# Kernel tuning notes

Hardware: AMD Instinct MI355X
Metric: run time of the kernel (lower is better)

Reference implementation:

```python
import jax, jax.numpy as jnp
import numpy as np

N = 50000   # nodes
E = 800000  # edges (avg degree 16)
IN = 3      # in_feats = value(1) + u(2)
H = 128     # hid_feats


def setup_inputs() -> dict:
    key = jax.random.key(0)
    ks = jax.random.split(key, 24)
    value = jax.random.normal(ks[0], (N, 1), jnp.float32)
    u = jax.random.normal(ks[1], (N, 2), jnp.float32)
    src = jax.random.randint(ks[2], (E,), 0, N, dtype=jnp.int32)
    dst = jax.random.randint(ks[3], (E,), 0, N, dtype=jnp.int32)
    dims = [IN, H // 2, H, H, H, H, H, H, H, H, 1]
    inp = {"value": value, "u": u, "src": src, "dst": dst}
    for i in range(10):
        inp[f"W{i+1}"] = jax.random.normal(ks[4 + i], (dims[i], dims[i + 1]), jnp.float32) / np.sqrt(dims[i]).astype(np.float32)
        inp[f"b{i+1}"] = jnp.zeros((dims[i + 1],), jnp.float32)
    return inp


def _gconv(x, src, dst, inv_deg, W, b):
    # DGL GraphConv norm='right': sum incoming src features, divide by in-degree, linear, bias
    agg = jax.ops.segment_sum(x[src], dst, num_segments=N)  # [N, d_in]
    return (agg * inv_deg) @ W + b


def reference(value, u, src, dst, W1, b1, W2, b2, W3, b3, W4, b4, W5, b5,
              W6, b6, W7, b7, W8, b8, W9, b9, W10, b10):
    deg = jax.ops.segment_sum(jnp.ones((E,), jnp.float32), dst, num_segments=N)
    inv_deg = (1.0 / jnp.clip(deg, 1.0))[:, None]  # DGL clamps in-degree to >=1
    lrelu = lambda h: jax.nn.leaky_relu(h, 0.01)
    x = jnp.concatenate([value, u], axis=1)  # [N, 3]
    h = _gconv(x, src, dst, inv_deg, W1, b1)
    h = lrelu(_gconv(h, src, dst, inv_deg, W2, b2))
    h = lrelu(_gconv(h, src, dst, inv_deg, W3, b3))
    h = lrelu(_gconv(h, src, dst, inv_deg, W4, b4))
    h = _gconv(h, src, dst, inv_deg, W5, b5)
    h = _gconv(h, src, dst, inv_deg, W6, b6)
    h = _gconv(h, src, dst, inv_deg, W7, b7)
    h = _gconv(h, src, dst, inv_deg, W8, b8)
    h = jax.nn.sigmoid(_gconv(h, src, dst, inv_deg, W9, b9))
    h = _gconv(h, src, dst, inv_deg, W10, b10)  # [N, 1]
    return h
```

## Files before the change

### kernel.cpp

```cpp
#include <hip/hip_runtime.h>
#include <math.h>

typedef unsigned int u32;
typedef unsigned short u16;
using bf16x8 = __attribute__((ext_vector_type(8))) short;
using f32x4 = __attribute__((ext_vector_type(4))) float;

__device__ inline float bf_lo(u32 v) { return __uint_as_float(v << 16); }
__device__ inline float bf_hi(u32 v) { return __uint_as_float(v & 0xFFFF0000u); }
__device__ inline u16 f2bf(float f) {
    u32 u = __float_as_uint(f);
    return (u16)((u + 0x7FFFu + ((u >> 16) & 1u)) >> 16);
}
__device__ inline float bf2f(u16 h) { return __uint_as_float((u32)h << 16); }
__device__ inline float invdeg(int d) { return 1.0f / (float)(d > 1 ? d : 1); }

#define BIN_SHIFT 13

__global__ __launch_bounds__(256) void k_scatter_seq(const int* __restrict__ src,
                                                     const int* __restrict__ dst,
                                                     int* __restrict__ cur,
                                                     u16* __restrict__ colp,
                                                     int E, int EB) {
    const int bin = blockIdx.x / EB;
    int e = (blockIdx.x - bin * EB) * 256 + threadIdx.x;
    if (e >= E) return;
    int d = dst[e];
    if ((d >> BIN_SHIFT) != bin) return;
    int slot = atomicAdd(&cur[d], 1);
    if (slot < 64) colp[(size_t)d * 64 + slot] = (u16)src[e];
}

__global__ __launch_bounds__(256) void k_x4(const float* __restrict__ value,
                                            const float* __restrict__ u,
                                            float4* __restrict__ x4, int n) {
    int i = blockIdx.x * 256 + threadIdx.x;
    if (i < n) x4[i] = make_float4(value[i], u[2 * i], u[2 * i + 1], 0.f);
}

struct W7 { const float* p[7]; };

__global__ __launch_bounds__(256) void k_pack(W7 wp, const float* __restrict__ W64,
                                              u16* __restrict__ hi128, u16* __restrict__ lo128,
                                              u16* __restrict__ hi64, u16* __restrict__ lo64) {
    const int l = blockIdx.y;
    if (l < 7) {
        const float* W = wp.p[l];
        int g = blockIdx.x * 256 + threadIdx.x;
        int ct = g >> 8;
        int rem = g & 255;
        int ks = rem >> 6;
        int lane = rem & 63;
        int kbase = ks * 32 + ((lane >> 4) << 3);
        int n = (ct << 4) + (lane & 15);
        size_t off = ((size_t)l * 2048 + g) * 8;
#pragma unroll
        for (int j = 0; j < 8; ++j) {
            float w = W[(size_t)(kbase + j) * 128 + n];
            u16 h = f2bf(w);
            hi128[off + j] = h;
            lo128[off + j] = f2bf(w - bf2f(h));
        }
    } else {
        if (blockIdx.x >= 4) return;
        int g = blockIdx.x * 256 + threadIdx.x;
        int ct = g >> 7;
        int rem = g & 127;
        int ks = rem >> 6;
        int lane = rem & 63;
        int kbase = ks * 32 + ((lane >> 4) << 3);
        int n = (ct << 4) + (lane & 15);
        size_t off = (size_t)g * 8;
#pragma unroll
        for (int j = 0; j < 8; ++j) {
            float w = W64[(size_t)(kbase + j) * 128 + n];
            u16 h = f2bf(w);
            hi64[off + j] = h;
            lo64[off + j] = f2bf(w - bf2f(h));
        }
    }
}

__global__ __launch_bounds__(256) void k_l1(const float4* __restrict__ x4,
                                            const u16* __restrict__ colp,
                                            const int* __restrict__ deg,
                                            const float* __restrict__ W1,
                                            const float* __restrict__ b1,
                                            u16* __restrict__ out, int nNodes) {
    const int lane = threadIdx.x & 63;
    const int n = blockIdx.x * 4 + (threadIdx.x >> 6);
    if (n >= nNodes) return;
    int dfull = deg[n];
    int dg = dfull > 64 ? 64 : dfull;
    const u16* cl = colp + (size_t)n * 64;
    float a0 = 0.f, a1 = 0.f, a2 = 0.f;
    if (lane < dg) {
        float4 v = x4[cl[lane]];
        a0 = v.x; a1 = v.y; a2 = v.z;
    }
#pragma unroll
    for (int o = 32; o; o >>= 1) {
        a0 += __shfl_xor(a0, o, 64);
        a1 += __shfl_xor(a1, o, 64);
        a2 += __shfl_xor(a2, o, 64);
    }
    float iv = invdeg(dfull);
    float y = b1[lane] + iv * (a0 * W1[lane] + a1 * W1[64 + lane] + a2 * W1[128 + lane]);
    out[(size_t)n * 64 + lane] = f2bf(y);
}

__global__ __launch_bounds__(256) void k_agg128b(const u32* __restrict__ H32,
                                                 const u16* __restrict__ colp,
                                                 const int* __restrict__ deg,
                                                 u32* __restrict__ out, int nNodes) {
    const int lane = threadIdx.x & 63;
    const int n = blockIdx.x * 4 + (threadIdx.x >> 6);
    if (n >= nNodes) return;
    int dfull = deg[n];
    int dg = dfull > 64 ? 64 : dfull;
    const u16* cl = colp + (size_t)n * 64;
    int myc = (lane < dg) ? (int)cl[lane] : 0;
    float a0 = 0.f, a1 = 0.f, b0 = 0.f, b1 = 0.f;
    int j = 0;
    for (; j + 8 <= dg; j += 8) {
        u32 v0 = H32[(size_t)__builtin_amdgcn_readlane(myc, j + 0) * 64 + lane];
        u32 v1 = H32[(size_t)__builtin_amdgcn_readlane(myc, j + 1) * 64 + lane];
        u32 v2 = H32[(size_t)__builtin_amdgcn_readlane(myc, j + 2) * 64 + lane];
        u32 v3 = H32[(size_t)__builtin_amdgcn_readlane(myc, j + 3) * 64 + lane];
        u32 v4 = H32[(size_t)__builtin_amdgcn_readlane(myc, j + 4) * 64 + lane];
        u32 v5 = H32[(size_t)__builtin_amdgcn_readlane(myc, j + 5) * 64 + lane];
        u32 v6 = H32[(size_t)__builtin_amdgcn_readlane(myc, j + 6) * 64 + lane];
        u32 v7 = H32[(size_t)__builtin_amdgcn_readlane(myc, j + 7) * 64 + lane];
        a0 += bf_lo(v0) + bf_lo(v1) + bf_lo(v2) + bf_lo(v3);
        a1 += bf_hi(v0) + bf_hi(v1) + bf_hi(v2) + bf_hi(v3);
        b0 += bf_lo(v4) + bf_lo(v5) + bf_lo(v6) + bf_lo(v7);
        b1 += bf_hi(v4) + bf_hi(v5) + bf_hi(v6) + bf_hi(v7);
    }
    for (; j + 4 <= dg; j += 4) {
        u32 v0 = H32[(size_t)__builtin_amdgcn_readlane(myc, j + 0) * 64 + lane];
        u32 v1 = H32[(size_t)__builtin_amdgcn_readlane(myc, j + 1) * 64 + lane];
        u32 v2 = H32[(size_t)__builtin_amdgcn_readlane(myc, j + 2) * 64 + lane];
        u32 v3 = H32[(size_t)__builtin_amdgcn_readlane(myc, j + 3) * 64 + lane];
        a0 += bf_lo(v0) + bf_lo(v1);
        a1 += bf_hi(v0) + bf_hi(v1);
        b0 += bf_lo(v2) + bf_lo(v3);
        b1 += bf_hi(v2) + bf_hi(v3);
    }
    for (; j < dg; ++j) {
        u32 v = H32[(size_t)__builtin_amdgcn_readlane(myc, j) * 64 + lane];
        a0 += bf_lo(v);
        a1 += bf_hi(v);
    }
    float iv = invdeg(dfull);
    out[(size_t)n * 64 + lane] =
        (u32)f2bf((a0 + b0) * iv) | ((u32)f2bf((a1 + b1) * iv) << 16);
}

__global__ __launch_bounds__(256) void k_agg64b(const u16* __restrict__ H16,
                                                const u16* __restrict__ colp,
                                                const int* __restrict__ deg,
                                                u16* __restrict__ out, int nNodes) {
    const int lane = threadIdx.x & 63;
    const int n = blockIdx.x * 4 + (threadIdx.x >> 6);
    if (n >= nNodes) return;
    int dfull = deg[n];
    int dg = dfull > 64 ? 64 : dfull;
    const u16* cl = colp + (size_t)n * 64;
    int myc = (lane < dg) ? (int)cl[lane] : 0;
    float a0 = 0.f, a1 = 0.f, b0 = 0.f, b1 = 0.f;
    int j = 0;
    for (; j + 8 <= dg; j += 8) {
        u16 v0 = H16[(size_t)__builtin_amdgcn_readlane(myc, j + 0) * 64 + lane];
        u16 v1 = H16[(size_t)__builtin_amdgcn_readlane(myc, j + 1) * 64 + lane];
        u16 v2 = H16[(size_t)__builtin_amdgcn_readlane(myc, j + 2) * 64 + lane];
        u16 v3 = H16[(size_t)__builtin_amdgcn_readlane(myc, j + 3) * 64 + lane];
        u16 v4 = H16[(size_t)__builtin_amdgcn_readlane(myc, j + 4) * 64 + lane];
        u16 v5 = H16[(size_t)__builtin_amdgcn_readlane(myc, j + 5) * 64 + lane];
        u16 v6 = H16[(size_t)__builtin_amdgcn_readlane(myc, j + 6) * 64 + lane];
        u16 v7 = H16[(size_t)__builtin_amdgcn_readlane(myc, j + 7) * 64 + lane];
        a0 += bf2f(v0) + bf2f(v1);
        a1 += bf2f(v2) + bf2f(v3);
        b0 += bf2f(v4) + bf2f(v5);
        b1 += bf2f(v6) + bf2f(v7);
    }
    for (; j + 4 <= dg; j += 4) {
        u16 v0 = H16[(size_t)__builtin_amdgcn_readlane(myc, j + 0) * 64 + lane];
        u16 v1 = H16[(size_t)__builtin_amdgcn_readlane(myc, j + 1) * 64 + lane];
        u16 v2 = H16[(size_t)__builtin_amdgcn_readlane(myc, j + 2) * 64 + lane];
        u16 v3 = H16[(size_t)__builtin_amdgcn_readlane(myc, j + 3) * 64 + lane];
        a0 += bf2f(v0) + bf2f(v1);
        b0 += bf2f(v2) + bf2f(v3);
    }
    for (; j < dg; ++j) {
        a0 += bf2f(H16[(size_t)__builtin_amdgcn_readlane(myc, j) * 64 + lane]);
    }
    out[(size_t)n * 64 + lane] = f2bf((a0 + a1 + b0 + b1) * invdeg(dfull));
}

template <int ACT>
__device__ inline float actf(float x) {
    if (ACT == 1) return x > 0.f ? x : 0.01f * x;
    if (ACT == 2) return 1.f / (1.f + expf(-x));
    return x;
}

template <int DIN, int ACT>
__global__ __launch_bounds__(256) void k_mm(const u16* __restrict__ A,
                                            const u16* __restrict__ pkHi,
                                            const u16* __restrict__ pkLo,
                                            const float* __restrict__ B,
                                            u16* __restrict__ Y, int nNodes) {
    constexpr int NKS = DIN / 32;
    const int lane = threadIdx.x & 63;
    const int w = threadIdx.x >> 6;
    const int base = blockIdx.x * 64 + w * 16;
    const int m = lane & 15;
    const int kb = lane >> 4;
    int arow = base + m;
    if (arow >= nNodes) arow = nNodes - 1;

    bf16x8 aF[NKS];
#pragma unroll
    for (int ks = 0; ks < NKS; ++ks)
        aF[ks] = *reinterpret_cast<const bf16x8*>(A + (size_t)arow * DIN + ks * 32 + kb * 8);

    const bf16x8* bh = reinterpret_cast<const bf16x8*>(pkHi);
    const bf16x8* bl = reinterpret_cast<const bf16x8*>(pkLo);

#pragma unroll
    for (int ct = 0; ct < 8; ++ct) {
        f32x4 acc = {0.f, 0.f, 0.f, 0.f};
#pragma unroll
        for (int ks = 0; ks < NKS; ++ks) {
            acc = __builtin_amdgcn_mfma_f32_16x16x32_bf16(aF[ks], bh[(ct * NKS + ks) * 64 + lane], acc, 0, 0, 0);
            acc = __builtin_amdgcn_mfma_f32_16x16x32_bf16(aF[ks], bl[(ct * NKS + ks) * 64 + lane], acc, 0, 0, 0);
        }
        float bias = B[ct * 16 + m];
#pragma unroll
        for (int r = 0; r < 4; ++r) {
            int row = base + kb * 4 + r;
            if (row < nNodes)
                Y[(size_t)row * 128 + ct * 16 + m] = f2bf(actf<ACT>(acc[r] + bias));
        }
    }
}

__global__ __launch_bounds__(256) void k_mm_last(const u16* __restrict__ A,
                                                 const u16* __restrict__ pkHi,
                                                 const u16* __restrict__ pkLo,
                                                 const float* __restrict__ B,
                                                 const float* __restrict__ w10,
                                                 float* __restrict__ t, int nNodes) {
    const int lane = threadIdx.x & 63;
    const int w = threadIdx.x >> 6;
    const int base = blockIdx.x * 64 + w * 16;
    const int m = lane & 15;
    const int kb = lane >> 4;
    int arow = base + m;
    if (arow >= nNodes) arow = nNodes - 1;

    bf16x8 aF[4];
#pragma unroll
    for (int ks = 0; ks < 4; ++ks)
        aF[ks] = *reinterpret_cast<const bf16x8*>(A + (size_t)arow * 128 + ks * 32 + kb * 8);

    const bf16x8* bh = reinterpret_cast<const bf16x8*>(pkHi);
    const bf16x8* bl = reinterpret_cast<const bf16x8*>(pkLo);

    float p0 = 0.f, p1 = 0.f, p2 = 0.f, p3 = 0.f;
#pragma unroll
    for (int ct = 0; ct < 8; ++ct) {
        f32x4 acc = {0.f, 0.f, 0.f, 0.f};
#pragma unroll
        for (int ks = 0; ks < 4; ++ks) {
            acc = __builtin_amdgcn_mfma_f32_16x16x32_bf16(aF[ks], bh[(ct * 4 + ks) * 64 + lane], acc, 0, 0, 0);
            acc = __builtin_amdgcn_mfma_f32_16x16x32_bf16(aF[ks], bl[(ct * 4 + ks) * 64 + lane], acc, 0, 0, 0);
        }
        float bias = B[ct * 16 + m];
        float wv = w10[ct * 16 + m];
        p0 += wv * actf<2>(acc[0] + bias);
        p1 += wv * actf<2>(acc[1] + bias);
        p2 += wv * actf<2>(acc[2] + bias);
        p3 += wv * actf<2>(acc[3] + bias);
    }
#pragma unroll
    for (int o = 1; o < 16; o <<= 1) {
        p0 += __shfl_xor(p0, o, 64);
        p1 += __shfl_xor(p1, o, 64);
        p2 += __shfl_xor(p2, o, 64);
        p3 += __shfl_xor(p3, o, 64);
    }
    if (m == 0) {
        int r0 = base + kb * 4;
        if (r0 + 0 < nNodes) t[r0 + 0] = p0;
        if (r0 + 1 < nNodes) t[r0 + 1] = p1;
        if (r0 + 2 < nNodes) t[r0 + 2] = p2;
        if (r0 + 3 < nNodes) t[r0 + 3] = p3;
    }
}

__global__ __launch_bounds__(256) void k_aggs(const float* __restrict__ t,
                                              const u16* __restrict__ colp,
                                              const int* __restrict__ deg,
                                              const float* __restrict__ B,
                                              float* __restrict__ out, int nNodes) {
    int n = blockIdx.x * 256 + threadIdx.x;
    if (n >= nNodes) return;
    int dfull = deg[n];
    int dg = dfull > 64 ? 64 : dfull;
    const u16* cl = colp + (size_t)n * 64;
    float s = 0.f;
    for (int j = 0; j < dg; ++j) s += t[cl[j]];
    out[n] = s * invdeg(dfull) + B[0];
}

extern "C" void kernel_launch(void* const* d_in, const int* in_sizes, int n_in,
                              void* d_out, int out_size, void* d_ws, size_t ws_size,
                              hipStream_t stream) {
    const float* value = (const float*)d_in[0];
    const float* u = (const float*)d_in[1];
    const int* src = (const int*)d_in[2];
    const int* dst = (const int*)d_in[3];
    const float* W[10];
    const float* b[10];
    for (int i = 0; i < 10; ++i) {
        W[i] = (const float*)d_in[4 + 2 * i];
        b[i] = (const float*)d_in[5 + 2 * i];
    }
    const int N = in_sizes[0];
    const int E = in_sizes[2];
    float* out = (float*)d_out;

    char* p = (char*)d_ws;
    auto carve = [&](size_t bytes) {
        char* r = p;
        p += (bytes + 255) & ~(size_t)255;
        return r;
    };
    int* deg = (int*)carve((size_t)N * 4);
    u16* colp = (u16*)carve((size_t)N * 64 * 2);
    float4* x4 = (float4*)carve((size_t)N * 16);
    u16* hA = (u16*)carve((size_t)N * 128 * 2);
    u16* hB = (u16*)carve((size_t)N * 128 * 2);
    u16* agg = (u16*)carve((size_t)N * 128 * 2);
    float* t10 = (float*)carve((size_t)N * 4);
    u16* pk128hi = (u16*)carve((size_t)7 * 2048 * 8 * 2);
    u16* pk128lo = (u16*)carve((size_t)7 * 2048 * 8 * 2);
    u16* pk64hi = (u16*)carve((size_t)1024 * 8 * 2);
    u16* pk64lo = (u16*)carve((size_t)1024 * 8 * 2);

    const int nbins = (N + (1 << BIN_SHIFT) - 1) >> BIN_SHIFT;
    const int EB = (E + 255) / 256;

    hipMemsetAsync(deg, 0, (size_t)N * 4, stream);
    k_scatter_seq<<<EB * nbins, 256, 0, stream>>>(src, dst, deg, colp, E, EB);
    k_x4<<<(N + 255) / 256, 256, 0, stream>>>(value, u, x4, N);

    W7 wp;
    for (int i = 0; i < 7; ++i) wp.p[i] = W[2 + i];
    k_pack<<<dim3(8, 8), 256, 0, stream>>>(wp, W[1], pk128hi, pk128lo, pk64hi, pk64lo);

    const int gw = (N + 3) / 4;
    const int gg = (N + 63) / 64;
    const int gt = (N + 255) / 256;
    const size_t PK = 2048 * 8;

    k_l1<<<gw, 256, 0, stream>>>(x4, colp, deg, W[0], b[0], hA, N);
    k_agg64b<<<gw, 256, 0, stream>>>(hA, colp, deg, agg, N);
    k_mm<64, 1><<<gg, 256, 0, stream>>>(agg, pk64hi, pk64lo, b[1], hB, N);
    k_agg128b<<<gw, 256, 0, stream>>>((const u32*)hB, colp, deg, (u32*)agg, N);
    k_mm<128, 1><<<gg, 256, 0, stream>>>(agg, pk128hi + 0 * PK, pk128lo + 0 * PK, b[2], hA, N);
    k_agg128b<<<gw, 256, 0, stream>>>((const u32*)hA, colp, deg, (u32*)agg, N);
    k_mm<128, 1><<<gg, 256, 0, stream>>>(agg, pk128hi + 1 * PK, pk128lo + 1 * PK, b[3], hB, N);
    k_agg128b<<<gw, 256, 0, stream>>>((const u32*)hB, colp, deg, (u32*)agg, N);
    k_mm<128, 0><<<gg, 256, 0, stream>>>(agg, pk128hi + 2 * PK, pk128lo + 2 * PK, b[4], hA, N);
    k_agg128b<<<gw, 256, 0, stream>>>((const u32*)hA, colp, deg, (u32*)agg, N);
    k_mm<128, 0><<<gg, 256, 0, stream>>>(agg, pk128hi + 3 * PK, pk128lo + 3 * PK, b[5], hB, N);
    k_agg128b<<<gw, 256, 0, stream>>>((const u32*)hB, colp, deg, (u32*)agg, N);
    k_mm<128, 0><<<gg, 256, 0, stream>>>(agg, pk128hi + 4 * PK, pk128lo + 4 * PK, b[6], hA, N);
    k_agg128b<<<gw, 256, 0, stream>>>((const u32*)hA, colp, deg, (u32*)agg, N);
    k_mm<128, 0><<<gg, 256, 0, stream>>>(agg, pk128hi + 5 * PK, pk128lo + 5 * PK, b[7], hB, N);
    k_agg128b<<<gw, 256, 0, stream>>>((const u32*)hB, colp, deg, (u32*)agg, N);
    k_mm_last<<<gg, 256, 0, stream>>>(agg, pk128hi + 6 * PK, pk128lo + 6 * PK, b[8], W[9], t10, N);
    k_aggs<<<gt, 256, 0, stream>>>(t10, colp, deg, b[9], out, N);
}
```

Before: 427.1 us.

## Fuse neighbor aggregation with MFMA matmul per 64-node tile and merge setup kernels

Each hidden layer now runs one 1024-thread block per 64-node tile. The block gathers and averages the neighbor features into the shared agg buffer, synchronises, then runs the split-bf16 MFMA matmul, with each wave computing two output column tiles. The edge scatter, input packing and weight packing kernels are merged into one front kernel to cut launches. The fused kernel still writes agg to global memory and reads it back after the block barrier, so traffic is barely reduced. It also puts a barrier between the gather and matmul phases, which limits overlap inside a block.

```diff
diff --git a/kernel.cpp b/kernel.cpp
--- a/kernel.cpp
+++ b/kernel.cpp
@@ -17,63 +17,67 @@
 
 #define BIN_SHIFT 13
 
-__global__ __launch_bounds__(256) void k_scatter_seq(const int* __restrict__ src,
-                                                     const int* __restrict__ dst,
-                                                     int* __restrict__ cur,
-                                                     u16* __restrict__ colp,
-                                                     int E, int EB) {
-    const int bin = blockIdx.x / EB;
-    int e = (blockIdx.x - bin * EB) * 256 + threadIdx.x;
-    if (e >= E) return;
-    int d = dst[e];
-    if ((d >> BIN_SHIFT) != bin) return;
-    int slot = atomicAdd(&cur[d], 1);
-    if (slot < 64) colp[(size_t)d * 64 + slot] = (u16)src[e];
-}
-
-__global__ __launch_bounds__(256) void k_x4(const float* __restrict__ value,
-                                            const float* __restrict__ u,
-                                            float4* __restrict__ x4, int n) {
-    int i = blockIdx.x * 256 + threadIdx.x;
-    if (i < n) x4[i] = make_float4(value[i], u[2 * i], u[2 * i + 1], 0.f);
-}
-
 struct W7 { const float* p[7]; };
 
-__global__ __launch_bounds__(256) void k_pack(W7 wp, const float* __restrict__ W64,
-                                              u16* __restrict__ hi128, u16* __restrict__ lo128,
-                                              u16* __restrict__ hi64, u16* __restrict__ lo64) {
-    const int l = blockIdx.y;
-    if (l < 7) {
+__global__ __launch_bounds__(256) void k_front(const int* __restrict__ src,
+                                               const int* __restrict__ dst,
+                                               int* __restrict__ cur,
+                                               u16* __restrict__ colp,
+                                               int E, int EB, int SB,
+                                               const float* __restrict__ value,
+                                               const float* __restrict__ u,
+                                               float4* __restrict__ x4, int n, int NBx4,
+                                               W7 wp, const float* __restrict__ W64,
+                                               u16* __restrict__ hi128, u16* __restrict__ lo128,
+                                               u16* __restrict__ hi64, u16* __restrict__ lo64) {
+    int blk = blockIdx.x;
+    if (blk < SB) {
+        const int bin = blk / EB;
+        int e = (blk - bin * EB) * 256 + threadIdx.x;
+        if (e >= E) return;
+        int d = dst[e];
+        if ((d >> BIN_SHIFT) != bin) return;
+        int slot = atomicAdd(&cur[d], 1);
+        if (slot < 64) colp[(size_t)d * 64 + slot] = (u16)src[e];
+        return;
+    }
+    int pb = blk - SB;
+    if (pb < NBx4) {
+        int i = pb * 256 + threadIdx.x;
+        if (i < n) x4[i] = make_float4(value[i], u[2 * i], u[2 * i + 1], 0.f);
+        return;
+    }
+    pb -= NBx4;
+    if (pb < 56) {
+        const int l = pb >> 3;
         const float* W = wp.p[l];
-        int g = blockIdx.x * 256 + threadIdx.x;
+        int g = (pb & 7) * 256 + threadIdx.x;
         int ct = g >> 8;
         int rem = g & 255;
         int ks = rem >> 6;
         int lane = rem & 63;
         int kbase = ks * 32 + ((lane >> 4) << 3);
-        int n = (ct << 4) + (lane & 15);
+        int nn = (ct << 4) + (lane & 15);
         size_t off = ((size_t)l * 2048 + g) * 8;
 #pragma unroll
         for (int j = 0; j < 8; ++j) {
-            float w = W[(size_t)(kbase + j) * 128 + n];
+            float w = W[(size_t)(kbase + j) * 128 + nn];
             u16 h = f2bf(w);
             hi128[off + j] = h;
             lo128[off + j] = f2bf(w - bf2f(h));
         }
     } else {
-        if (blockIdx.x >= 4) return;
-        int g = blockIdx.x * 256 + threadIdx.x;
+        int g = (pb - 56) * 256 + threadIdx.x;
         int ct = g >> 7;
         int rem = g & 127;
         int ks = rem >> 6;
         int lane = rem & 63;
         int kbase = ks * 32 + ((lane >> 4) << 3);
-        int n = (ct << 4) + (lane & 15);
+        int nn = (ct << 4) + (lane & 15);
         size_t off = (size_t)g * 8;
 #pragma unroll
         for (int j = 0; j < 8; ++j) {
-            float w = W64[(size_t)(kbase + j) * 128 + n];
+            float w = W64[(size_t)(kbase + j) * 128 + nn];
             u16 h = f2bf(w);
             hi64[off + j] = h;
             lo64[off + j] = f2bf(w - bf2f(h));
@@ -109,6 +113,147 @@
     out[(size_t)n * 64 + lane] = f2bf(y);
 }
 
+template <int ACT>
+__device__ inline float actf(float x) {
+    if (ACT == 1) return x > 0.f ? x : 0.01f * x;
+    if (ACT == 2) return 1.f / (1.f + expf(-x));
+    return x;
+}
+
+template <int DIN>
+__device__ inline void agg_node(const void* __restrict__ Hin, const u16* __restrict__ colp,
+                                const int* __restrict__ deg, u16* __restrict__ aggbuf,
+                                int n, int lane) {
+    int dfull = deg[n];
+    int dg = dfull > 64 ? 64 : dfull;
+    const u16* cl = colp + (size_t)n * 64;
+    int myc = (lane < dg) ? (int)cl[lane] : 0;
+    if (DIN == 128) {
+        const u32* H32 = (const u32*)Hin;
+        float a0 = 0.f, a1 = 0.f, b0 = 0.f, b1 = 0.f;
+        int j = 0;
+        for (; j + 8 <= dg; j += 8) {
+            u32 v0 = H32[(size_t)__builtin_amdgcn_readlane(myc, j + 0) * 64 + lane];
+            u32 v1 = H32[(size_t)__builtin_amdgcn_readlane(myc, j + 1) * 64 + lane];
+            u32 v2 = H32[(size_t)__builtin_amdgcn_readlane(myc, j + 2) * 64 + lane];
+            u32 v3 = H32[(size_t)__builtin_amdgcn_readlane(myc, j + 3) * 64 + lane];
+            u32 v4 = H32[(size_t)__builtin_amdgcn_readlane(myc, j + 4) * 64 + lane];
+            u32 v5 = H32[(size_t)__builtin_amdgcn_readlane(myc, j + 5) * 64 + lane];
+            u32 v6 = H32[(size_t)__builtin_amdgcn_readlane(myc, j + 6) * 64 + lane];
+            u32 v7 = H32[(size_t)__builtin_amdgcn_readlane(myc, j + 7) * 64 + lane];
+            a0 += bf_lo(v0) + bf_lo(v1) + bf_lo(v2) + bf_lo(v3);
+            a1 += bf_hi(v0) + bf_hi(v1) + bf_hi(v2) + bf_hi(v3);
+            b0 += bf_lo(v4) + bf_lo(v5) + bf_lo(v6) + bf_lo(v7);
+            b1 += bf_hi(v4) + bf_hi(v5) + bf_hi(v6) + bf_hi(v7);
+        }
+        for (; j + 4 <= dg; j += 4) {
+            u32 v0 = H32[(size_t)__builtin_amdgcn_readlane(myc, j + 0) * 64 + lane];
+            u32 v1 = H32[(size_t)__builtin_amdgcn_readlane(myc, j + 1) * 64 + lane];
+            u32 v2 = H32[(size_t)__builtin_amdgcn_readlane(myc, j + 2) * 64 + lane];
+            u32 v3 = H32[(size_t)__builtin_amdgcn_readlane(myc, j + 3) * 64 + lane];
+            a0 += bf_lo(v0) + bf_lo(v1);
+            a1 += bf_hi(v0) + bf_hi(v1);
+            b0 += bf_lo(v2) + bf_lo(v3);
+            b1 += bf_hi(v2) + bf_hi(v3);
+        }
+        for (; j < dg; ++j) {
+            u32 v = H32[(size_t)__builtin_amdgcn_readlane(myc, j) * 64 + lane];
+            a0 += bf_lo(v);
+            a1 += bf_hi(v);
+        }
+        float iv = invdeg(dfull);
+        ((u32*)aggbuf)[(size_t)n * 64 + lane] =
+            (u32)f2bf((a0 + b0) * iv) | ((u32)f2bf((a1 + b1) * iv) << 16);
+    } else {
+        const u16* H16 = (const u16*)Hin;
+        float a0 = 0.f, a1 = 0.f, b0 = 0.f, b1 = 0.f;
+        int j = 0;
+        for (; j + 8 <= dg; j += 8) {
+            u16 v0 = H16[(size_t)__builtin_amdgcn_readlane(myc, j + 0) * 64 + lane];
+            u16 v1 = H16[(size_t)__builtin_amdgcn_readlane(myc, j + 1) * 64 + lane];
+            u16 v2 = H16[(size_t)__builtin_amdgcn_readlane(myc, j + 2) * 64 + lane];
+            u16 v3 = H16[(size_t)__builtin_amdgcn_readlane(myc, j + 3) * 64 + lane];
+            u16 v4 = H16[(size_t)__builtin_amdgcn_readlane(myc, j + 4) * 64 + lane];
+            u16 v5 = H16[(size_t)__builtin_amdgcn_readlane(myc, j + 5) * 64 + lane];
+            u16 v6 = H16[(size_t)__builtin_amdgcn_readlane(myc, j + 6) * 64 + lane];
+            u16 v7 = H16[(size_t)__builtin_amdgcn_readlane(myc, j + 7) * 64 + lane];
+            a0 += bf2f(v0) + bf2f(v1);
+            a1 += bf2f(v2) + bf2f(v3);
+            b0 += bf2f(v4) + bf2f(v5);
+            b1 += bf2f(v6) + bf2f(v7);
+        }
+        for (; j + 4 <= dg; j += 4) {
+            u16 v0 = H16[(size_t)__builtin_amdgcn_readlane(myc, j + 0) * 64 + lane];
+            u16 v1 = H16[(size_t)__builtin_amdgcn_readlane(myc, j + 1) * 64 + lane];
+            u16 v2 = H16[(size_t)__builtin_amdgcn_readlane(myc, j + 2) * 64 + lane];
+            u16 v3 = H16[(size_t)__builtin_amdgcn_readlane(myc, j + 3) * 64 + lane];
+            a0 += bf2f(v0) + bf2f(v1);
+            b0 += bf2f(v2) + bf2f(v3);
+        }
+        for (; j < dg; ++j) {
+            a0 += bf2f(H16[(size_t)__builtin_amdgcn_readlane(myc, j) * 64 + lane]);
+        }
+        aggbuf[(size_t)n * 64 + lane] = f2bf((a0 + a1 + b0 + b1) * invdeg(dfull));
+    }
+}
+
+template <int DIN, int ACT>
+__global__ __launch_bounds__(1024, 8) void k_fuse(const void* __restrict__ Hin,
+                                                  const u16* __restrict__ colp,
+                                                  const int* __restrict__ deg,
+                                                  u16* __restrict__ aggbuf,
+                                                  const u16* __restrict__ pkHi,
+                                                  const u16* __restrict__ pkLo,
+                                                  const float* __restrict__ B,
+                                                  u16* __restrict__ Y, int nNodes) {
+    const int tid = threadIdx.x;
+    const int lane = tid & 63;
+    const int w = tid >> 6;
+    const int tile = blockIdx.x * 64;
+
+#pragma unroll
+    for (int i = 0; i < 4; ++i) {
+        int n = tile + w * 4 + i;
+        if (n < nNodes) agg_node<DIN>(Hin, colp, deg, aggbuf, n, lane);
+    }
+    __syncthreads();
+
+    constexpr int NKS = DIN / 32;
+    const int m = lane & 15;
+    const int kb = lane >> 4;
+    const int rg = w & 3;
+    const int ct0 = (w >> 2) * 2;
+    const int base = tile + rg * 16;
+    int arow = base + m;
+    if (arow >= nNodes) arow = nNodes - 1;
+
+    bf16x8 aF[NKS];
+#pragma unroll
+    for (int ks = 0; ks < NKS; ++ks)
+        aF[ks] = *reinterpret_cast<const bf16x8*>(aggbuf + (size_t)arow * DIN + ks * 32 + kb * 8);
+
+    const bf16x8* bh = reinterpret_cast<const bf16x8*>(pkHi);
+    const bf16x8* bl = reinterpret_cast<const bf16x8*>(pkLo);
+
+#pragma unroll
+    for (int c = 0; c < 2; ++c) {
+        const int ct = ct0 + c;
+        f32x4 acc = {0.f, 0.f, 0.f, 0.f};
+#pragma unroll
+        for (int ks = 0; ks < NKS; ++ks) {
+            acc = __builtin_amdgcn_mfma_f32_16x16x32_bf16(aF[ks], bh[(ct * NKS + ks) * 64 + lane], acc, 0, 0, 0);
+            acc = __builtin_amdgcn_mfma_f32_16x16x32_bf16(aF[ks], bl[(ct * NKS + ks) * 64 + lane], acc, 0, 0, 0);
+        }
+        float bias = B[ct * 16 + m];
+#pragma unroll
+        for (int r = 0; r < 4; ++r) {
+            int row = base + kb * 4 + r;
+            if (row < nNodes)
+                Y[(size_t)row * 128 + ct * 16 + m] = f2bf(actf<ACT>(acc[r] + bias));
+        }
+    }
+}
+
 __global__ __launch_bounds__(256) void k_agg128b(const u32* __restrict__ H32,
                                                  const u16* __restrict__ colp,
                                                  const int* __restrict__ deg,
@@ -116,133 +261,7 @@
     const int lane = threadIdx.x & 63;
     const int n = blockIdx.x * 4 + (threadIdx.x >> 6);
     if (n >= nNodes) return;
-    int dfull = deg[n];
-    int dg = dfull > 64 ? 64 : dfull;
-    const u16* cl = colp + (size_t)n * 64;
-    int myc = (lane < dg) ? (int)cl[lane] : 0;
-    float a0 = 0.f, a1 = 0.f, b0 = 0.f, b1 = 0.f;
-    int j = 0;
-    for (; j + 8 <= dg; j += 8) {
-        u32 v0 = H32[(size_t)__builtin_amdgcn_readlane(myc, j + 0) * 64 + lane];
-        u32 v1 = H32[(size_t)__builtin_amdgcn_readlane(myc, j + 1) * 64 + lane];
-        u32 v2 = H32[(size_t)__builtin_amdgcn_readlane(myc, j + 2) * 64 + lane];
-        u32 v3 = H32[(size_t)__builtin_amdgcn_readlane(myc, j + 3) * 64 + lane];
-        u32 v4 = H32[(size_t)__builtin_amdgcn_readlane(myc, j + 4) * 64 + lane];
-        u32 v5 = H32[(size_t)__builtin_amdgcn_readlane(myc, j + 5) * 64 + lane];
-        u32 v6 = H32[(size_t)__builtin_amdgcn_readlane(myc, j + 6) * 64 + lane];
-        u32 v7 = H32[(size_t)__builtin_amdgcn_readlane(myc, j + 7) * 64 + lane];
-        a0 += bf_lo(v0) + bf_lo(v1) + bf_lo(v2) + bf_lo(v3);
-        a1 += bf_hi(v0) + bf_hi(v1) + bf_hi(v2) + bf_hi(v3);
-        b0 += bf_lo(v4) + bf_lo(v5) + bf_lo(v6) + bf_lo(v7);
-        b1 += bf_hi(v4) + bf_hi(v5) + bf_hi(v6) + bf_hi(v7);
-    }
-    for (; j + 4 <= dg; j += 4) {
-        u32 v0 = H32[(size_t)__builtin_amdgcn_readlane(myc, j + 0) * 64 + lane];
-        u32 v1 = H32[(size_t)__builtin_amdgcn_readlane(myc, j + 1) * 64 + lane];
-        u32 v2 = H32[(size_t)__builtin_amdgcn_readlane(myc, j + 2) * 64 + lane];
-        u32 v3 = H32[(size_t)__builtin_amdgcn_readlane(myc, j + 3) * 64 + lane];
-        a0 += bf_lo(v0) + bf_lo(v1);
-        a1 += bf_hi(v0) + bf_hi(v1);
-        b0 += bf_lo(v2) + bf_lo(v3);
-        b1 += bf_hi(v2) + bf_hi(v3);
-    }
-    for (; j < dg; ++j) {
-        u32 v = H32[(size_t)__builtin_amdgcn_readlane(myc, j) * 64 + lane];
-        a0 += bf_lo(v);
-        a1 += bf_hi(v);
-    }
-    float iv = invdeg(dfull);
-    out[(size_t)n * 64 + lane] =
-        (u32)f2bf((a0 + b0) * iv) | ((u32)f2bf((a1 + b1) * iv) << 16);
-}
-
-__global__ __launch_bounds__(256) void k_agg64b(const u16* __restrict__ H16,
-                                                const u16* __restrict__ colp,
-                                                const int* __restrict__ deg,
-                                                u16* __restrict__ out, int nNodes) {
-    const int lane = threadIdx.x & 63;
-    const int n = blockIdx.x * 4 + (threadIdx.x >> 6);
-    if (n >= nNodes) return;
-    int dfull = deg[n];
-    int dg = dfull > 64 ? 64 : dfull;
-    const u16* cl = colp + (size_t)n * 64;
-    int myc = (lane < dg) ? (int)cl[lane] : 0;
-    float a0 = 0.f, a1 = 0.f, b0 = 0.f, b1 = 0.f;
-    int j = 0;
-    for (; j + 8 <= dg; j += 8) {
-        u16 v0 = H16[(size_t)__builtin_amdgcn_readlane(myc, j + 0) * 64 + lane];
-        u16 v1 = H16[(size_t)__builtin_amdgcn_readlane(myc, j + 1) * 64 + lane];
-        u16 v2 = H16[(size_t)__builtin_amdgcn_readlane(myc, j + 2) * 64 + lane];
-        u16 v3 = H16[(size_t)__builtin_amdgcn_readlane(myc, j + 3) * 64 + lane];
-        u16 v4 = H16[(size_t)__builtin_amdgcn_readlane(myc, j + 4) * 64 + lane];
-        u16 v5 = H16[(size_t)__builtin_amdgcn_readlane(myc, j + 5) * 64 + lane];
-        u16 v6 = H16[(size_t)__builtin_amdgcn_readlane(myc, j + 6) * 64 + lane];
-        u16 v7 = H16[(size_t)__builtin_amdgcn_readlane(myc, j + 7) * 64 + lane];
-        a0 += bf2f(v0) + bf2f(v1);
-        a1 += bf2f(v2) + bf2f(v3);
-        b0 += bf2f(v4) + bf2f(v5);
-        b1 += bf2f(v6) + bf2f(v7);
-    }
-    for (; j + 4 <= dg; j += 4) {
-        u16 v0 = H16[(size_t)__builtin_amdgcn_readlane(myc, j + 0) * 64 + lane];
-        u16 v1 = H16[(size_t)__builtin_amdgcn_readlane(myc, j + 1) * 64 + lane];
-        u16 v2 = H16[(size_t)__builtin_amdgcn_readlane(myc, j + 2) * 64 + lane];
-        u16 v3 = H16[(size_t)__builtin_amdgcn_readlane(myc, j + 3) * 64 + lane];
-        a0 += bf2f(v0) + bf2f(v1);
-        b0 += bf2f(v2) + bf2f(v3);
-    }
-    for (; j < dg; ++j) {
-        a0 += bf2f(H16[(size_t)__builtin_amdgcn_readlane(myc, j) * 64 + lane]);
-    }
-    out[(size_t)n * 64 + lane] = f2bf((a0 + a1 + b0 + b1) * invdeg(dfull));
-}
-
-template <int ACT>
-__device__ inline float actf(float x) {
-    if (ACT == 1) return x > 0.f ? x : 0.01f * x;
-    if (ACT == 2) return 1.f / (1.f + expf(-x));
-    return x;
-}
-
-template <int DIN, int ACT>
-__global__ __launch_bounds__(256) void k_mm(const u16* __restrict__ A,
-                                            const u16* __restrict__ pkHi,
-                                            const u16* __restrict__ pkLo,
-                                            const float* __restrict__ B,
-                                            u16* __restrict__ Y, int nNodes) {
-    constexpr int NKS = DIN / 32;
-    const int lane = threadIdx.x & 63;
-    const int w = threadIdx.x >> 6;
-    const int base = blockIdx.x * 64 + w * 16;
-    const int m = lane & 15;
-    const int kb = lane >> 4;
-    int arow = base + m;
-    if (arow >= nNodes) arow = nNodes - 1;
-
-    bf16x8 aF[NKS];
-#pragma unroll
-    for (int ks = 0; ks < NKS; ++ks)
-        aF[ks] = *reinterpret_cast<const bf16x8*>(A + (size_t)arow * DIN + ks * 32 + kb * 8);
-
-    const bf16x8* bh = reinterpret_cast<const bf16x8*>(pkHi);
-    const bf16x8* bl = reinterpret_cast<const bf16x8*>(pkLo);
-
-#pragma unroll
-    for (int ct = 0; ct < 8; ++ct) {
-        f32x4 acc = {0.f, 0.f, 0.f, 0.f};
-#pragma unroll
-        for (int ks = 0; ks < NKS; ++ks) {
-            acc = __builtin_amdgcn_mfma_f32_16x16x32_bf16(aF[ks], bh[(ct * NKS + ks) * 64 + lane], acc, 0, 0, 0);
-            acc = __builtin_amdgcn_mfma_f32_16x16x32_bf16(aF[ks], bl[(ct * NKS + ks) * 64 + lane], acc, 0, 0, 0);
-        }
-        float bias = B[ct * 16 + m];
-#pragma unroll
-        for (int r = 0; r < 4; ++r) {
-            int row = base + kb * 4 + r;
-            if (row < nNodes)
-                Y[(size_t)row * 128 + ct * 16 + m] = f2bf(actf<ACT>(acc[r] + bias));
-        }
-    }
+    agg_node<128>((const void*)H32, colp, deg, (u16*)out, n, lane);
 }
 
 __global__ __launch_bounds__(256) void k_mm_last(const u16* __restrict__ A,
@@ -351,36 +370,31 @@
 
     const int nbins = (N + (1 << BIN_SHIFT) - 1) >> BIN_SHIFT;
     const int EB = (E + 255) / 256;
+    const int SB = EB * nbins;
+    const int NBx4 = (N + 255) / 256;
 
     hipMemsetAsync(deg, 0, (size_t)N * 4, stream);
-    k_scatter_seq<<<EB * nbins, 256, 0, stream>>>(src, dst, deg, colp, E, EB);
-    k_x4<<<(N + 255) / 256, 256, 0, stream>>>(value, u, x4, N);
 
     W7 wp;
     for (int i = 0; i < 7; ++i) wp.p[i] = W[2 + i];
-    k_pack<<<dim3(8, 8), 256, 0, stream>>>(wp, W[1], pk128hi, pk128lo, pk64hi, pk64lo);
+    k_front<<<SB + NBx4 + 60, 256, 0, stream>>>(src, dst, deg, colp, E, EB, SB,
+                                                value, u, x4, N, NBx4, wp, W[1],
+                                                pk128hi, pk128lo, pk64hi, pk64lo);
 
     const int gw = (N + 3) / 4;
-    const int gg = (N + 63) / 64;
+    const int gf = (N + 63) / 64;
     const int gt = (N + 255) / 256;
     const size_t PK = 2048 * 8;
 
     k_l1<<<gw, 256, 0, stream>>>(x4, colp, deg, W[0], b[0], hA, N);
-    k_agg64b<<<gw, 256, 0, stream>>>(hA, colp, deg, agg, N);
-    k_mm<64, 1><<<gg, 256, 0, stream>>>(agg, pk64hi, pk64lo, b[1], hB, N);
+    k_fuse<64, 1><<<gf, 1024, 0, stream>>>(hA, colp, deg, agg, pk64hi, pk64lo, b[1], hB, N);
+    k_fuse<128, 1><<<gf, 1024, 0, stream>>>(hB, colp, deg, agg, pk128hi + 0 * PK, pk128lo + 0 * PK, b[2], hA, N);
+    k_fuse<128, 1><<<gf, 1024, 0, stream>>>(hA, colp, deg, agg, pk128hi + 1 * PK, pk128lo + 1 * PK, b[3], hB, N);
+    k_fuse<128, 0><<<gf, 1024, 0, stream>>>(hB, colp, deg, agg, pk128hi + 2 * PK, pk128lo + 2 * PK, b[4], hA, N);
+    k_fuse<128, 0><<<gf, 1024, 0, stream>>>(hA, colp, deg, agg, pk128hi + 3 * PK, pk128lo + 3 * PK, b[5], hB, N);
+    k_fuse<128, 0><<<gf, 1024, 0, stream>>>(hB, colp, deg, agg, pk128hi + 4 * PK, pk128lo + 4 * PK, b[6], hA, N);
+    k_fuse<128, 0><<<gf, 1024, 0, stream>>>(hA, colp, deg, agg, pk128hi + 5 * PK, pk128lo + 5 * PK, b[7], hB, N);
     k_agg128b<<<gw, 256, 0, stream>>>((const u32*)hB, colp, deg, (u32*)agg, N);
-    k_mm<128, 1><<<gg, 256, 0, stream>>>(agg, pk128hi + 0 * PK, pk128lo + 0 * PK, b[2], hA, N);
-    k_agg128b<<<gw, 256, 0, stream>>>((const u32*)hA, colp, deg, (u32*)agg, N);
-    k_mm<128, 1><<<gg, 256, 0, stream>>>(agg, pk128hi + 1 * PK, pk128lo + 1 * PK, b[3], hB, N);
-    k_agg128b<<<gw, 256, 0, stream>>>((const u32*)hB, colp, deg, (u32*)agg, N);
-    k_mm<128, 0><<<gg, 256, 0, stream>>>(agg, pk128hi + 2 * PK, pk128lo + 2 * PK, b[4], hA, N);
-    k_agg128b<<<gw, 256, 0, stream>>>((const u32*)hA, colp, deg, (u32*)agg, N);
-    k_mm<128, 0><<<gg, 256, 0, stream>>>(agg, pk128hi + 3 * PK, pk128lo + 3 * PK, b[5], hB, N);
-    k_agg128b<<<gw, 256, 0, stream>>>((const u32*)hB, colp, deg, (u32*)agg, N);
-    k_mm<128, 0><<<gg, 256, 0, stream>>>(agg, pk128hi + 4 * PK, pk128lo + 4 * PK, b[6], hA, N);
-    k_agg128b<<<gw, 256, 0, stream>>>((const u32*)hA, colp, deg, (u32*)agg, N);
-    k_mm<128, 0><<<gg, 256, 0, stream>>>(agg, pk128hi + 5 * PK, pk128lo + 5 * PK, b[7], hB, N);
-    k_agg128b<<<gw, 256, 0, stream>>>((const u32*)hB, colp, deg, (u32*)agg, N);
-    k_mm_last<<<gg, 256, 0, stream>>>(agg, pk128hi + 6 * PK, pk128lo + 6 * PK, b[8], W[9], t10, N);
+    k_mm_last<<<gf, 256, 0, stream>>>(agg, pk128hi + 6 * PK, pk128lo + 6 * PK, b[8], W[9], t10, N);
     k_aggs<<<gt, 256, 0, stream>>>(t10, colp, deg, b[9], out, N);
 }
```

Result: slower. 442.6 us (+3.6%).
